# Performance work log

Measured on AMD Instinct MI355X. Metric: run time of the kernel, lower is better.

Reference implementation:

```python
import jax, jax.numpy as jnp
import numpy as np

B = 1024        # num samples
D = 1024        # feature dim d = DIM * K_RANK
K_RANK = 16     # data_object.k (low rank)
DIM = 64        # d / k
N_CLASSES = 10
L = 16          # residual layers


def setup_inputs() -> dict:
    key = jax.random.key(0)
    ks = jax.random.split(key, 7)
    X = jax.random.normal(ks[0], (B, 3, D), jnp.float32)
    W0 = jax.random.normal(ks[1], (D, D), jnp.float32) / np.sqrt(D).astype(np.float32)
    Ws = jax.random.normal(ks[2], (L, D, D), jnp.float32) / np.sqrt(D).astype(np.float32)
    bs = jax.random.normal(ks[3], (L, D), jnp.float32) * 0.01
    Wc = jax.random.normal(ks[4], (N_CLASSES, DIM * DIM), jnp.float32) / np.sqrt(DIM * DIM).astype(np.float32)
    bc = jax.random.normal(ks[5], (N_CLASSES,), jnp.float32) * 0.01
    h = jnp.full((1,), 1.0 / L, jnp.float32)  # trainable stepsize, init 1/L
    return {"X": X, "h": h, "W0": W0, "Ws": Ws, "bs": bs, "Wc": Wc, "bc": bc}


def _polar(A):
    # polar projection onto Stiefel: U[:, :, :k] @ Vh[:, :k, :] == reduced U @ Vh
    U, S, Vh = jnp.linalg.svd(A, full_matrices=False)
    return U @ Vh


def _project_svd(X):
    # X: (B, 3, D); channels = (U_tilde, S, V_tilde), each matrix is (DIM, K_RANK)
    U = _polar(X[:, 0].reshape(-1, DIM, K_RANK))
    V = _polar(X[:, 2].reshape(-1, DIM, K_RANK))
    return jnp.stack([U.reshape(-1, D), X[:, 1], V.reshape(-1, D)], axis=1)


def reference(X, h, W0, Ws, bs, Wc, bc):
    # preprocessing: vh stored row-major as (k, dim) -> v = vh^T flattened
    v = jnp.swapaxes(X[:, 2].reshape(-1, K_RANK, DIM), 1, 2).reshape(-1, D)
    X = jnp.stack([X[:, 0], X[:, 1], v], axis=1)  # (B, 3, D)

    # layer 0: Linear without bias, then Stiefel projection
    X = _project_svd(jnp.einsum('bcd,ed->bce', X, W0))
    xs = [X]

    # residual layers: X <- Proj(X + h * relu(Linear(X)))
    for i in range(L):
        Y = X + h[0] * jax.nn.relu(jnp.einsum('bcd,ed->bce', X, Ws[i]) + bs[i])
        X = _project_svd(Y)
        xs.append(X)

    X_transformed = jnp.stack(xs, axis=-1)  # (B, 3, D, L+1)

    # reconstruct: U @ S[:k,:k] @ V^T, then classify
    U = X[:, 0].reshape(-1, DIM, K_RANK)
    S = X[:, 1].reshape(-1, DIM, K_RANK)[:, :K_RANK, :K_RANK]
    V = X[:, 2].reshape(-1, DIM, K_RANK)
    Z = (U @ S @ jnp.swapaxes(V, 1, 2)).reshape(-1, DIM * DIM)
    X_classified = Z @ Wc.T + bc
    X_predicted = jax.nn.softmax(X_classified, axis=1)
    return X_predicted, X_classified, X_transformed
```

## Files before the change

### kernel.cpp

```cpp
#include <hip/hip_runtime.h>
#include <hip/hip_bf16.h>

#define DD    1024
#define NROWS 3072
#define NLAY  17
#define MS    20

typedef __attribute__((ext_vector_type(8))) short short8;
typedef __attribute__((ext_vector_type(4))) float floatx4;

__global__ __launch_bounds__(256) void convw_kernel(const float* __restrict__ W0,
                                                    const float* __restrict__ Ws,
                                                    ushort* __restrict__ Wbf) {
  const size_t i4 = ((size_t)blockIdx.x * 256 + threadIdx.x) * 4;
  float4 v;
  if (i4 < 1048576) v = *(const float4*)(W0 + i4);
  else              v = *(const float4*)(Ws + (i4 - 1048576));
  union { __hip_bfloat16 h[4]; ushort u[4]; } pk;
  pk.h[0] = __float2bfloat16(v.x); pk.h[1] = __float2bfloat16(v.y);
  pk.h[2] = __float2bfloat16(v.z); pk.h[3] = __float2bfloat16(v.w);
  *(ushort4*)(Wbf + i4) = *(ushort4*)pk.u;
}

__global__ __launch_bounds__(256) void prep_kernel(const float* __restrict__ Xin,
                                                   ushort* __restrict__ X0bf) {
  const int row = blockIdx.x;
  const int c   = row % 3;
  const float* src = Xin + (size_t)row * DD;
  ushort* dst = X0bf + (size_t)row * DD;
  for (int t = threadIdx.x; t < DD; t += 256) {
    float v;
    if (c == 2) v = src[(t & 15) * 64 + (t >> 4)];
    else        v = src[t];
    __hip_bfloat16 h = __float2bfloat16(v);
    dst[t] = *(ushort*)&h;
  }
}

__global__ __launch_bounds__(256) void gemm_kernel(
    const ushort* __restrict__ Abf, const ushort* __restrict__ Wbf,
    const float* __restrict__ Xres, const float* __restrict__ bias,
    const float* __restrict__ hp, float* __restrict__ Y, int fuse)
{
  __shared__ __align__(16) ushort As[128 * 32];
  __shared__ __align__(16) ushort Bs[64 * 32];
  const int tid  = threadIdx.x;
  const int wave = tid >> 6, lane = tid & 63;

  const int id = blockIdx.x;
  const int w  = (id & 7) * 48 + (id >> 3);
  const int bm = (w >> 4) * 128;
  const int bn = (w & 15) * 64;

  const int srow = wave * 16 + (lane >> 2);
  const int scol = (lane & 3) * 8;
  const ushort* ga0 = Abf + (size_t)(bm + srow) * DD + scol;
  const ushort* gb0 = Wbf + (size_t)(bn + srow) * DD + scol;

  const int wm0 = (wave >> 1) * 64, wn0 = (wave & 1) * 32;
  const int m = lane & 15, quad = lane >> 4;

  floatx4 acc[4][2] = {};

  for (int k0 = 0; k0 < DD; k0 += 32) {
    __syncthreads();
#pragma unroll
    for (int q = 0; q < 2; ++q) {
      __builtin_amdgcn_global_load_lds(
          (const __attribute__((address_space(1))) unsigned int*)(ga0 + (size_t)q * 64 * DD + k0),
          (__attribute__((address_space(3))) unsigned int*)&As[(q * 64 + wave * 16) * 32],
          16, 0, 0);
    }
    __builtin_amdgcn_global_load_lds(
        (const __attribute__((address_space(1))) unsigned int*)(gb0 + k0),
        (__attribute__((address_space(3))) unsigned int*)&Bs[(wave * 16) * 32],
        16, 0, 0);
    __syncthreads();

    short8 av[4], bv[2];
#pragma unroll
    for (int i = 0; i < 4; ++i)
      av[i] = *(const short8*)&As[(wm0 + i * 16 + m) * 32 + quad * 8];
#pragma unroll
    for (int j = 0; j < 2; ++j)
      bv[j] = *(const short8*)&Bs[(wn0 + j * 16 + m) * 32 + quad * 8];
#pragma unroll
    for (int i = 0; i < 4; ++i)
#pragma unroll
      for (int j = 0; j < 2; ++j)
        acc[i][j] = __builtin_amdgcn_mfma_f32_16x16x32_bf16(av[i], bv[j], acc[i][j], 0, 0, 0);
  }

  const float h = fuse ? hp[0] : 0.0f;
#pragma unroll
  for (int i = 0; i < 4; ++i) {
#pragma unroll
    for (int r = 0; r < 4; ++r) {
      const int grow = bm + wm0 + i * 16 + quad * 4 + r;
      float* yr = Y + (size_t)grow * DD;
      const float* xr = Xres + (size_t)grow * DD;
#pragma unroll
      for (int j = 0; j < 2; ++j) {
        const int gcol = bn + wn0 + j * 16 + m;
        float d = acc[i][j][r];
        if (fuse) d = xr[gcol] + h * fmaxf(d + bias[gcol], 0.0f);
        yr[gcol] = d;
      }
    }
  }
}

__global__ __launch_bounds__(64) void proj_kernel(
    const float* __restrict__ Yg, float* __restrict__ Xg,
    __hip_bfloat16* __restrict__ stage, int layer, int iters)
{
  __shared__ float At[16 * 68];
  __shared__ __align__(16) float Yb[16 * MS];
  __shared__ __align__(16) float Zb[16 * MS];
  __shared__ __align__(16) float Tb[16 * MS];

  const int lane = threadIdx.x;

  if (blockIdx.x >= 2048) {
    const int b = blockIdx.x - 2048;
    const int row = b * 3 + 1;
    const float* src = Yg + (size_t)row * DD + lane * 16;
    float* dst = Xg + (size_t)row * DD + lane * 16;
    float v[16];
#pragma unroll
    for (int q = 0; q < 4; ++q) {
      const float4 t4 = *(const float4*)(src + q * 4);
      v[q*4+0]=t4.x; v[q*4+1]=t4.y; v[q*4+2]=t4.z; v[q*4+3]=t4.w;
      *(float4*)(dst + q * 4) = t4;
    }
    union { __hip_bfloat16 hh[16]; uint4 u[2]; } pk;
#pragma unroll
    for (int j = 0; j < 16; ++j) pk.hh[j] = __float2bfloat16(v[j]);
    uint4* sd = (uint4*)(stage + ((size_t)layer * NROWS + row) * DD + lane * 16);
    sd[0] = pk.u[0]; sd[1] = pk.u[1];
    return;
  }

  const int p = blockIdx.x;
  const int b = p >> 1;
  const int row = b * 3 + (p & 1) * 2;
  const float* src = Yg + (size_t)row * DD + lane * 16;

  float v[16];
#pragma unroll
  for (int q = 0; q < 4; ++q) {
    const float4 t4 = *(const float4*)(src + q * 4);
    v[q*4+0]=t4.x; v[q*4+1]=t4.y; v[q*4+2]=t4.z; v[q*4+3]=t4.w;
  }
  float f2 = 0.f;
#pragma unroll
  for (int j = 0; j < 16; ++j) f2 += v[j] * v[j];
#pragma unroll
  for (int o = 32; o > 0; o >>= 1) f2 += __shfl_xor(f2, o, 64);
  const float s = rsqrtf(f2 + 1e-30f);
#pragma unroll
  for (int j = 0; j < 16; ++j) v[j] *= s;

#pragma unroll
  for (int j = 0; j < 16; ++j) At[j * 68 + lane] = v[j];
  __syncthreads();

  const int fc = lane & 15, fq = lane >> 4;
  short8 fa, fb;
  {
    const float* rp = &At[fc * 68 + fq * 8];
    const float4 a0 = *(const float4*)(rp + 0);
    const float4 a1 = *(const float4*)(rp + 4);
    const float4 b0 = *(const float4*)(rp + 32);
    const float4 b1 = *(const float4*)(rp + 36);
    union { __hip_bfloat16 h[8]; short8 s8; } pa, pb;
    pa.h[0]=__float2bfloat16(a0.x); pa.h[1]=__float2bfloat16(a0.y);
    pa.h[2]=__float2bfloat16(a0.z); pa.h[3]=__float2bfloat16(a0.w);
    pa.h[4]=__float2bfloat16(a1.x); pa.h[5]=__float2bfloat16(a1.y);
    pa.h[6]=__float2bfloat16(a1.z); pa.h[7]=__float2bfloat16(a1.w);
    pb.h[0]=__float2bfloat16(b0.x); pb.h[1]=__float2bfloat16(b0.y);
    pb.h[2]=__float2bfloat16(b0.z); pb.h[3]=__float2bfloat16(b0.w);
    pb.h[4]=__float2bfloat16(b1.x); pb.h[5]=__float2bfloat16(b1.y);
    pb.h[6]=__float2bfloat16(b1.z); pb.h[7]=__float2bfloat16(b1.w);
    fa = pa.s8; fb = pb.s8;
  }
  floatx4 gacc = {};
  gacc = __builtin_amdgcn_mfma_f32_16x16x32_bf16(fa, fa, gacc, 0, 0, 0);
  gacc = __builtin_amdgcn_mfma_f32_16x16x32_bf16(fb, fb, gacc, 0, 0, 0);

  float ss = gacc[0]*gacc[0] + gacc[1]*gacc[1] + gacc[2]*gacc[2] + gacc[3]*gacc[3];
#pragma unroll
  for (int o = 32; o > 0; o >>= 1) ss += __shfl_xor(ss, o, 64);
  const float gf = rsqrtf(ss + 1e-30f);

#pragma unroll
  for (int j = 0; j < 4; ++j) Yb[(fq * 4 + j) * MS + fc] = gacc[j] * gf;
  const int r  = lane >> 2;
  const int c0 = (lane & 3) * 4;
  *(float4*)&Zb[r * MS + c0] = make_float4(r == c0+0 ? 1.f : 0.f,
                                           r == c0+1 ? 1.f : 0.f,
                                           r == c0+2 ? 1.f : 0.f,
                                           r == c0+3 ? 1.f : 0.f);
  __syncthreads();

  for (int it = 0; it < iters; ++it) {
    float zr[16], yr[16];
    {
      const float4 za = *(const float4*)&Zb[r * MS + 0];
      const float4 zb4 = *(const float4*)&Zb[r * MS + 4];
      const float4 zc = *(const float4*)&Zb[r * MS + 8];
      const float4 zd = *(const float4*)&Zb[r * MS + 12];
      zr[0]=za.x; zr[1]=za.y; zr[2]=za.z; zr[3]=za.w;
      zr[4]=zb4.x; zr[5]=zb4.y; zr[6]=zb4.z; zr[7]=zb4.w;
      zr[8]=zc.x; zr[9]=zc.y; zr[10]=zc.z; zr[11]=zc.w;
      zr[12]=zd.x; zr[13]=zd.y; zr[14]=zd.z; zr[15]=zd.w;
      const float4 ya = *(const float4*)&Yb[r * MS + 0];
      const float4 yb4 = *(const float4*)&Yb[r * MS + 4];
      const float4 yc = *(const float4*)&Yb[r * MS + 8];
      const float4 yd = *(const float4*)&Yb[r * MS + 12];
      yr[0]=ya.x; yr[1]=ya.y; yr[2]=ya.z; yr[3]=ya.w;
      yr[4]=yb4.x; yr[5]=yb4.y; yr[6]=yb4.z; yr[7]=yb4.w;
      yr[8]=yc.x; yr[9]=yc.y; yr[10]=yc.z; yr[11]=yc.w;
      yr[12]=yd.x; yr[13]=yd.y; yr[14]=yd.z; yr[15]=yd.w;
    }
    float p0=0.f, p1=0.f, p2=0.f, p3=0.f;
#pragma unroll
    for (int k = 0; k < 16; ++k) {
      const float4 y4 = *(const float4*)&Yb[k * MS + c0];
      p0 = fmaf(zr[k], y4.x, p0); p1 = fmaf(zr[k], y4.y, p1);
      p2 = fmaf(zr[k], y4.z, p2); p3 = fmaf(zr[k], y4.w, p3);
    }
    float4 tv;
    tv.x = 0.5f * ((r == c0+0 ? 3.f : 0.f) - p0);
    tv.y = 0.5f * ((r == c0+1 ? 3.f : 0.f) - p1);
    tv.z = 0.5f * ((r == c0+2 ? 3.f : 0.f) - p2);
    tv.w = 0.5f * ((r == c0+3 ? 3.f : 0.f) - p3);
    *(float4*)&Tb[r * MS + c0] = tv;
    __syncthreads();
    float4 py = make_float4(0,0,0,0), pz = make_float4(0,0,0,0);
#pragma unroll
    for (int k = 0; k < 16; ++k) {
      const float4 t4 = *(const float4*)&Tb[k * MS + c0];
      py.x = fmaf(yr[k], t4.x, py.x); py.y = fmaf(yr[k], t4.y, py.y);
      py.z = fmaf(yr[k], t4.z, py.z); py.w = fmaf(yr[k], t4.w, py.w);
      pz.x = fmaf(zr[k], t4.x, pz.x); pz.y = fmaf(zr[k], t4.y, pz.y);
      pz.z = fmaf(zr[k], t4.z, pz.z); pz.w = fmaf(zr[k], t4.w, pz.w);
    }
    *(float4*)&Yb[r * MS + c0] = py;
    *(float4*)&Zb[r * MS + c0] = pz;
    __syncthreads();
  }

  const float us = sqrtf(gf);
#pragma unroll
  for (int j = 0; j < 16; ++j) v[j] *= us;

  float up[16] = {};
#pragma unroll
  for (int k = 0; k < 16; ++k) {
    const float a = v[k];
#pragma unroll
    for (int j0 = 0; j0 < 16; j0 += 4) {
      const float4 z4 = *(const float4*)&Zb[k * MS + j0];
      up[j0+0] = fmaf(a, z4.x, up[j0+0]);
      up[j0+1] = fmaf(a, z4.y, up[j0+1]);
      up[j0+2] = fmaf(a, z4.z, up[j0+2]);
      up[j0+3] = fmaf(a, z4.w, up[j0+3]);
    }
  }
  float* dst = Xg + (size_t)row * DD + lane * 16;
#pragma unroll
  for (int q = 0; q < 4; ++q)
    *(float4*)(dst + q*4) = make_float4(up[q*4], up[q*4+1], up[q*4+2], up[q*4+3]);
  union { __hip_bfloat16 hh[16]; uint4 u[2]; } pk;
#pragma unroll
  for (int j = 0; j < 16; ++j) pk.hh[j] = __float2bfloat16(up[j]);
  uint4* sd = (uint4*)(stage + ((size_t)layer * NROWS + row) * DD + lane * 16);
  sd[0] = pk.u[0]; sd[1] = pk.u[1];
}

__global__ __launch_bounds__(256) void transpose_kernel(
    const __hip_bfloat16* __restrict__ stage, float* __restrict__ outT)
{
  __shared__ float buf[256 * 18];
  const int row = blockIdx.y;
  const int d0  = blockIdx.x * 256;
  const int t   = threadIdx.x;
  for (int l = 0; l < NLAY; ++l)
    buf[t * 18 + l] = __bfloat162float(stage[((size_t)l * NROWS + row) * DD + d0 + t]);
  __syncthreads();
  const size_t ob = (size_t)(row * DD + d0) * NLAY;
  for (int i = 0; i < NLAY; ++i) {
    const int idx = i * 256 + t;
    const int dd = idx / 17, ll = idx % 17;
    outT[ob + idx] = buf[dd * 18 + ll];
  }
}

__global__ __launch_bounds__(256) void classify_kernel(
    const float* __restrict__ X, const float* __restrict__ Wc,
    const float* __restrict__ bc, float* __restrict__ out)
{
  __shared__ float U[64*17], S[16*17], V[64*17], T[64*17];
  __shared__ float Z[4096];
  __shared__ float wsum[4][10];
  const int b = blockIdx.x, t = threadIdx.x;
  const float* x0 = X + (size_t)(b*3+0) * DD;
  const float* x1 = X + (size_t)(b*3+1) * DD;
  const float* x2 = X + (size_t)(b*3+2) * DD;
  for (int e = t; e < 1024; e += 256) {
    const int i = e >> 4, j = e & 15;
    U[i*17+j] = x0[e];
    V[i*17+j] = x2[e];
  }
  { const int i = t >> 4, j = t & 15; if (t < 256) S[i*17+j] = x1[i*16+j]; }
  __syncthreads();
  for (int e = t; e < 1024; e += 256) {
    const int i = e >> 4, j = e & 15;
    float a = 0.f;
    for (int k = 0; k < 16; ++k) a = fmaf(U[i*17+k], S[k*17+j], a);
    T[i*17+j] = a;
  }
  __syncthreads();
  for (int e = t; e < 4096; e += 256) {
    const int i = e >> 6, j = e & 63;
    float a = 0.f;
    for (int k = 0; k < 16; ++k) a = fmaf(T[i*17+k], V[j*17+k], a);
    Z[e] = a;
  }
  __syncthreads();
  float part[10] = {};
  for (int e = t; e < 4096; e += 256) {
    const float z = Z[e];
#pragma unroll
    for (int n = 0; n < 10; ++n) part[n] = fmaf(z, Wc[(size_t)n * 4096 + e], part[n]);
  }
#pragma unroll
  for (int n = 0; n < 10; ++n) {
#pragma unroll
    for (int off = 32; off > 0; off >>= 1) part[n] += __shfl_xor(part[n], off, 64);
  }
  if ((t & 63) == 0) {
#pragma unroll
    for (int n = 0; n < 10; ++n) wsum[t >> 6][n] = part[n];
  }
  __syncthreads();
  if (t == 0) {
    float logits[10];
#pragma unroll
    for (int n = 0; n < 10; ++n)
      logits[n] = wsum[0][n] + wsum[1][n] + wsum[2][n] + wsum[3][n] + bc[n];
    float mx = logits[0];
    for (int n = 1; n < 10; ++n) mx = fmaxf(mx, logits[n]);
    float ex[10], sm = 0.f;
    for (int n = 0; n < 10; ++n) { ex[n] = expf(logits[n] - mx); sm += ex[n]; }
    const float inv = 1.f / sm;
    for (int n = 0; n < 10; ++n) {
      out[b*10 + n] = ex[n] * inv;
      out[10240 + b*10 + n] = logits[n];
    }
  }
}

extern "C" void kernel_launch(void* const* d_in, const int* in_sizes, int n_in,
                              void* d_out, int out_size, void* d_ws, size_t ws_size,
                              hipStream_t stream) {
  const float* Xin = (const float*)d_in[0];
  const float* hp  = (const float*)d_in[1];
  const float* W0  = (const float*)d_in[2];
  const float* Ws  = (const float*)d_in[3];
  const float* bs  = (const float*)d_in[4];
  const float* Wc  = (const float*)d_in[5];
  const float* bc  = (const float*)d_in[6];
  float* out = (float*)d_out;

  char* ws = (char*)d_ws;
  float* Xb = (float*)ws;
  float* Yb = Xb + (size_t)NROWS * DD;
  __hip_bfloat16* stage =
      (__hip_bfloat16*)(ws + 2 * (size_t)NROWS * DD * 4);
  ushort* X0bf = (ushort*)(ws + 2 * (size_t)NROWS * DD * 4
                              + (size_t)NLAY * NROWS * DD * 2);
  ushort* Wbf  = X0bf + (size_t)NROWS * DD;

  convw_kernel<<<17408, 256, 0, stream>>>(W0, Ws, Wbf);
  prep_kernel<<<NROWS, 256, 0, stream>>>(Xin, X0bf);

  gemm_kernel<<<384, 256, 0, stream>>>(X0bf, Wbf, Xb, bs, hp, Yb, 0);
  proj_kernel<<<3072, 64, 0, stream>>>(Yb, Xb, stage, 0, 13);

  for (int l = 0; l < 16; ++l) {
    gemm_kernel<<<384, 256, 0, stream>>>(
        (const ushort*)(stage + (size_t)l * NROWS * DD),
        Wbf + (size_t)(l + 1) * DD * DD,
        Xb, bs + (size_t)l * DD, hp, Yb, 1);
    proj_kernel<<<3072, 64, 0, stream>>>(Yb, Xb, stage, l + 1, 9);
  }

  transpose_kernel<<<dim3(4, NROWS), 256, 0, stream>>>(stage, out + 20480);
  classify_kernel<<<1024, 256, 0, stream>>>(Xb, Wc, bc, out);
}
```

Baseline: 1.069 ms.

## Run Newton-Schulz polar iterations on MFMA with split-bf16 precision

Replaces the scalar FMA 16x16 matrix products in the Newton-Schulz polar iteration, and the final A·Z product, with MFMA bf16 instructions. Each fp32 operand is split into high and low bf16 parts and combined with three MFMAs to recover near-fp32 accuracy. Shared-memory syncthreads are replaced by compiler memory barriers, since a single wavefront owns each block. This cuts VALU work and barriers per iteration, but adds split/convert overhead and LDS round-trips to rebuild fragment layouts.

Result: faster. 1.004 ms (-6.1%).

```diff
diff --git a/kernel.cpp b/kernel.cpp
--- a/kernel.cpp
+++ b/kernel.cpp
@@ -110,14 +110,26 @@
   }
 }
 
+__device__ __forceinline__ void split_wr(ushort* Bh, ushort* Bl, int c, int q, floatx4 a) {
+  union { ushort u[4]; uint2 d; } ph, pl;
+#pragma unroll
+  for (int j = 0; j < 4; ++j) {
+    const float x = a[j];
+    __hip_bfloat16 hb = __float2bfloat16(x);
+    const float hf = __bfloat162float(hb);
+    __hip_bfloat16 lb = __float2bfloat16(x - hf);
+    ph.u[j] = *(const ushort*)&hb;
+    pl.u[j] = *(const ushort*)&lb;
+  }
+  *(uint2*)&Bh[c * 40 + q * 4] = ph.d;
+  *(uint2*)&Bl[c * 40 + q * 4] = pl.d;
+}
+
 __global__ __launch_bounds__(64) void proj_kernel(
     const float* __restrict__ Yg, float* __restrict__ Xg,
     __hip_bfloat16* __restrict__ stage, int layer, int iters)
 {
-  __shared__ float At[16 * 68];
-  __shared__ __align__(16) float Yb[16 * MS];
-  __shared__ __align__(16) float Zb[16 * MS];
-  __shared__ __align__(16) float Tb[16 * MS];
+  __shared__ __align__(16) ushort POOL[5632];
 
   const int lane = threadIdx.x;
 
@@ -152,121 +164,139 @@
     const float4 t4 = *(const float4*)(src + q * 4);
     v[q*4+0]=t4.x; v[q*4+1]=t4.y; v[q*4+2]=t4.z; v[q*4+3]=t4.w;
   }
-  float f2 = 0.f;
-#pragma unroll
-  for (int j = 0; j < 16; ++j) f2 += v[j] * v[j];
-#pragma unroll
-  for (int o = 32; o > 0; o >>= 1) f2 += __shfl_xor(f2, o, 64);
-  const float s = rsqrtf(f2 + 1e-30f);
+  float nrm = 0.f;
+#pragma unroll
+  for (int j = 0; j < 16; ++j) nrm += v[j] * v[j];
+#pragma unroll
+  for (int o = 32; o > 0; o >>= 1) nrm += __shfl_xor(nrm, o, 64);
+  const float s = rsqrtf(nrm + 1e-30f);
 #pragma unroll
   for (int j = 0; j < 16; ++j) v[j] *= s;
 
-#pragma unroll
-  for (int j = 0; j < 16; ++j) At[j * 68 + lane] = v[j];
-  __syncthreads();
-
-  const int fc = lane & 15, fq = lane >> 4;
-  short8 fa, fb;
-  {
-    const float* rp = &At[fc * 68 + fq * 8];
-    const float4 a0 = *(const float4*)(rp + 0);
-    const float4 a1 = *(const float4*)(rp + 4);
-    const float4 b0 = *(const float4*)(rp + 32);
-    const float4 b1 = *(const float4*)(rp + 36);
-    union { __hip_bfloat16 h[8]; short8 s8; } pa, pb;
-    pa.h[0]=__float2bfloat16(a0.x); pa.h[1]=__float2bfloat16(a0.y);
-    pa.h[2]=__float2bfloat16(a0.z); pa.h[3]=__float2bfloat16(a0.w);
-    pa.h[4]=__float2bfloat16(a1.x); pa.h[5]=__float2bfloat16(a1.y);
-    pa.h[6]=__float2bfloat16(a1.z); pa.h[7]=__float2bfloat16(a1.w);
-    pb.h[0]=__float2bfloat16(b0.x); pb.h[1]=__float2bfloat16(b0.y);
-    pb.h[2]=__float2bfloat16(b0.z); pb.h[3]=__float2bfloat16(b0.w);
-    pb.h[4]=__float2bfloat16(b1.x); pb.h[5]=__float2bfloat16(b1.y);
-    pb.h[6]=__float2bfloat16(b1.z); pb.h[7]=__float2bfloat16(b1.w);
-    fa = pa.s8; fb = pb.s8;
-  }
+  ushort* ATl = POOL;
+  ushort* Bh  = POOL + 1152;
+  ushort* Bl  = POOL + 1792;
+  const int fr = lane & 15, fq = lane >> 4;
+
+#pragma unroll
+  for (int j = 0; j < 16; ++j) {
+    __hip_bfloat16 hb = __float2bfloat16(v[j]);
+    ATl[j * 72 + lane] = *(const ushort*)&hb;
+  }
+  *(uint2*)&Bh[fr * 40 + 16 + fq * 4] = make_uint2(0u, 0u);
+  *(uint2*)&Bl[fr * 40 + 16 + fq * 4] = make_uint2(0u, 0u);
+  asm volatile("" ::: "memory");
+
+  short8 g1 = *(const short8*)&ATl[fr * 72 + fq * 8];
+  short8 g2 = *(const short8*)&ATl[fr * 72 + 32 + fq * 8];
   floatx4 gacc = {};
-  gacc = __builtin_amdgcn_mfma_f32_16x16x32_bf16(fa, fa, gacc, 0, 0, 0);
-  gacc = __builtin_amdgcn_mfma_f32_16x16x32_bf16(fb, fb, gacc, 0, 0, 0);
+  gacc = __builtin_amdgcn_mfma_f32_16x16x32_bf16(g1, g1, gacc, 0, 0, 0);
+  gacc = __builtin_amdgcn_mfma_f32_16x16x32_bf16(g2, g2, gacc, 0, 0, 0);
 
   float ss = gacc[0]*gacc[0] + gacc[1]*gacc[1] + gacc[2]*gacc[2] + gacc[3]*gacc[3];
 #pragma unroll
   for (int o = 32; o > 0; o >>= 1) ss += __shfl_xor(ss, o, 64);
   const float gf = rsqrtf(ss + 1e-30f);
 
-#pragma unroll
-  for (int j = 0; j < 4; ++j) Yb[(fq * 4 + j) * MS + fc] = gacc[j] * gf;
-  const int r  = lane >> 2;
-  const int c0 = (lane & 3) * 4;
-  *(float4*)&Zb[r * MS + c0] = make_float4(r == c0+0 ? 1.f : 0.f,
-                                           r == c0+1 ? 1.f : 0.f,
-                                           r == c0+2 ? 1.f : 0.f,
-                                           r == c0+3 ? 1.f : 0.f);
-  __syncthreads();
+  floatx4 yd;
+#pragma unroll
+  for (int j = 0; j < 4; ++j) yd[j] = gacc[j] * gf;
+  split_wr(Bh, Bl, fr, fq, yd);
+  asm volatile("" ::: "memory");
+  short8 Yh = *(const short8*)&Bh[fr * 40 + fq * 8];
+  short8 Yl = *(const short8*)&Bl[fr * 40 + fq * 8];
+  short8 Zh, Zl;
+#pragma unroll
+  for (int d = 0; d < 8; ++d) {
+    Zh[d] = (fr == fq * 8 + d) ? (short)0x3F80 : (short)0;
+    Zl[d] = 0;
+  }
 
   for (int it = 0; it < iters; ++it) {
-    float zr[16], yr[16];
-    {
-      const float4 za = *(const float4*)&Zb[r * MS + 0];
-      const float4 zb4 = *(const float4*)&Zb[r * MS + 4];
-      const float4 zc = *(const float4*)&Zb[r * MS + 8];
-      const float4 zd = *(const float4*)&Zb[r * MS + 12];
-      zr[0]=za.x; zr[1]=za.y; zr[2]=za.z; zr[3]=za.w;
-      zr[4]=zb4.x; zr[5]=zb4.y; zr[6]=zb4.z; zr[7]=zb4.w;
-      zr[8]=zc.x; zr[9]=zc.y; zr[10]=zc.z; zr[11]=zc.w;
-      zr[12]=zd.x; zr[13]=zd.y; zr[14]=zd.z; zr[15]=zd.w;
-      const float4 ya = *(const float4*)&Yb[r * MS + 0];
-      const float4 yb4 = *(const float4*)&Yb[r * MS + 4];
-      const float4 yc = *(const float4*)&Yb[r * MS + 8];
-      const float4 yd = *(const float4*)&Yb[r * MS + 12];
-      yr[0]=ya.x; yr[1]=ya.y; yr[2]=ya.z; yr[3]=ya.w;
-      yr[4]=yb4.x; yr[5]=yb4.y; yr[6]=yb4.z; yr[7]=yb4.w;
-      yr[8]=yc.x; yr[9]=yc.y; yr[10]=yc.z; yr[11]=yc.w;
-      yr[12]=yd.x; yr[13]=yd.y; yr[14]=yd.z; yr[15]=yd.w;
-    }
-    float p0=0.f, p1=0.f, p2=0.f, p3=0.f;
-#pragma unroll
-    for (int k = 0; k < 16; ++k) {
-      const float4 y4 = *(const float4*)&Yb[k * MS + c0];
-      p0 = fmaf(zr[k], y4.x, p0); p1 = fmaf(zr[k], y4.y, p1);
-      p2 = fmaf(zr[k], y4.z, p2); p3 = fmaf(zr[k], y4.w, p3);
-    }
-    float4 tv;
-    tv.x = 0.5f * ((r == c0+0 ? 3.f : 0.f) - p0);
-    tv.y = 0.5f * ((r == c0+1 ? 3.f : 0.f) - p1);
-    tv.z = 0.5f * ((r == c0+2 ? 3.f : 0.f) - p2);
-    tv.w = 0.5f * ((r == c0+3 ? 3.f : 0.f) - p3);
-    *(float4*)&Tb[r * MS + c0] = tv;
-    __syncthreads();
-    float4 py = make_float4(0,0,0,0), pz = make_float4(0,0,0,0);
-#pragma unroll
-    for (int k = 0; k < 16; ++k) {
-      const float4 t4 = *(const float4*)&Tb[k * MS + c0];
-      py.x = fmaf(yr[k], t4.x, py.x); py.y = fmaf(yr[k], t4.y, py.y);
-      py.z = fmaf(yr[k], t4.z, py.z); py.w = fmaf(yr[k], t4.w, py.w);
-      pz.x = fmaf(zr[k], t4.x, pz.x); pz.y = fmaf(zr[k], t4.y, pz.y);
-      pz.z = fmaf(zr[k], t4.z, pz.z); pz.w = fmaf(zr[k], t4.w, pz.w);
-    }
-    *(float4*)&Yb[r * MS + c0] = py;
-    *(float4*)&Zb[r * MS + c0] = pz;
-    __syncthreads();
+    floatx4 wv = {};
+    wv = __builtin_amdgcn_mfma_f32_16x16x32_bf16(Zh, Yh, wv, 0, 0, 0);
+    wv = __builtin_amdgcn_mfma_f32_16x16x32_bf16(Zh, Yl, wv, 0, 0, 0);
+    wv = __builtin_amdgcn_mfma_f32_16x16x32_bf16(Zl, Yh, wv, 0, 0, 0);
+    floatx4 td;
+#pragma unroll
+    for (int j = 0; j < 4; ++j)
+      td[j] = ((fq * 4 + j == fr) ? 1.5f : 0.f) - 0.5f * wv[j];
+    split_wr(Bh, Bl, fr, fq, td);
+    asm volatile("" ::: "memory");
+    short8 Th = *(const short8*)&Bh[fr * 40 + fq * 8];
+    short8 Tl = *(const short8*)&Bl[fr * 40 + fq * 8];
+    floatx4 zd = {};
+    zd = __builtin_amdgcn_mfma_f32_16x16x32_bf16(Zh, Th, zd, 0, 0, 0);
+    zd = __builtin_amdgcn_mfma_f32_16x16x32_bf16(Zh, Tl, zd, 0, 0, 0);
+    zd = __builtin_amdgcn_mfma_f32_16x16x32_bf16(Zl, Th, zd, 0, 0, 0);
+    if (it < iters - 1) {
+      floatx4 yn = {};
+      yn = __builtin_amdgcn_mfma_f32_16x16x32_bf16(Yh, Th, yn, 0, 0, 0);
+      yn = __builtin_amdgcn_mfma_f32_16x16x32_bf16(Yh, Tl, yn, 0, 0, 0);
+      yn = __builtin_amdgcn_mfma_f32_16x16x32_bf16(Yl, Th, yn, 0, 0, 0);
+      split_wr(Bh, Bl, fr, fq, yn);
+      asm volatile("" ::: "memory");
+      Yh = *(const short8*)&Bh[fr * 40 + fq * 8];
+      Yl = *(const short8*)&Bl[fr * 40 + fq * 8];
+    }
+    split_wr(Bh, Bl, fr, fq, zd);
+    asm volatile("" ::: "memory");
+    Zh = *(const short8*)&Bh[fr * 40 + fq * 8];
+    Zl = *(const short8*)&Bl[fr * 40 + fq * 8];
   }
 
   const float us = sqrtf(gf);
-#pragma unroll
-  for (int j = 0; j < 16; ++j) v[j] *= us;
-
-  float up[16] = {};
-#pragma unroll
-  for (int k = 0; k < 16; ++k) {
-    const float a = v[k];
-#pragma unroll
-    for (int j0 = 0; j0 < 16; j0 += 4) {
-      const float4 z4 = *(const float4*)&Zb[k * MS + j0];
-      up[j0+0] = fmaf(a, z4.x, up[j0+0]);
-      up[j0+1] = fmaf(a, z4.y, up[j0+1]);
-      up[j0+2] = fmaf(a, z4.z, up[j0+2]);
-      up[j0+3] = fmaf(a, z4.w, up[j0+3]);
-    }
+  asm volatile("" ::: "memory");
+  ushort* Ah = POOL;
+  ushort* Al = POOL + 2560;
+  {
+    union { ushort u[16]; uint4 q4[2]; } rh, rl;
+#pragma unroll
+    for (int j = 0; j < 16; ++j) {
+      const float x = v[j] * us;
+      __hip_bfloat16 hb = __float2bfloat16(x);
+      const float hf = __bfloat162float(hb);
+      __hip_bfloat16 lb = __float2bfloat16(x - hf);
+      rh.u[j] = *(const ushort*)&hb;
+      rl.u[j] = *(const ushort*)&lb;
+    }
+    *(uint4*)&Ah[lane * 40]      = rh.q4[0];
+    *(uint4*)&Ah[lane * 40 + 8]  = rh.q4[1];
+    *(uint4*)&Al[lane * 40]      = rl.q4[0];
+    *(uint4*)&Al[lane * 40 + 8]  = rl.q4[1];
+    const uint4 zz = make_uint4(0u, 0u, 0u, 0u);
+    *(uint4*)&Ah[lane * 40 + 16] = zz; *(uint4*)&Ah[lane * 40 + 24] = zz;
+    *(uint4*)&Al[lane * 40 + 16] = zz; *(uint4*)&Al[lane * 40 + 24] = zz;
+  }
+  asm volatile("" ::: "memory");
+  short8 ah[4], al[4];
+#pragma unroll
+  for (int m4 = 0; m4 < 4; ++m4) {
+    ah[m4] = *(const short8*)&Ah[(m4 * 16 + fr) * 40 + fq * 8];
+    al[m4] = *(const short8*)&Al[(m4 * 16 + fr) * 40 + fq * 8];
+  }
+  floatx4 um[4];
+#pragma unroll
+  for (int m4 = 0; m4 < 4; ++m4) {
+    floatx4 a = {};
+    a = __builtin_amdgcn_mfma_f32_16x16x32_bf16(ah[m4], Zh, a, 0, 0, 0);
+    a = __builtin_amdgcn_mfma_f32_16x16x32_bf16(ah[m4], Zl, a, 0, 0, 0);
+    a = __builtin_amdgcn_mfma_f32_16x16x32_bf16(al[m4], Zh, a, 0, 0, 0);
+    um[m4] = a;
+  }
+  asm volatile("" ::: "memory");
+  float* Ub = (float*)POOL;
+#pragma unroll
+  for (int m4 = 0; m4 < 4; ++m4)
+#pragma unroll
+    for (int j = 0; j < 4; ++j)
+      Ub[(m4 * 16 + fq * 4 + j) * 20 + fr] = um[m4][j];
+  asm volatile("" ::: "memory");
+  float up[16];
+#pragma unroll
+  for (int i = 0; i < 4; ++i) {
+    const float4 t4 = *(const float4*)&Ub[lane * 20 + i * 4];
+    up[i*4+0]=t4.x; up[i*4+1]=t4.y; up[i*4+2]=t4.z; up[i*4+3]=t4.w;
   }
   float* dst = Xg + (size_t)row * DD + lane * 16;
 #pragma unroll
```
